# Performance work log

Hardware: AMD Instinct MI355X
Metric: run time of the kernel (lower is better)

The kernel has to match this reference:

```python
import jax, jax.numpy as jnp
import numpy as np

B, S, D = 2, 2048, 1024
H, HD = 16, 64  # num heads, head dim
EPS = 1e-12
SCALING = HD ** -0.5


def rotate_half(x):
    x1, x2 = jnp.split(x, 2, axis=-1)
    return jnp.concatenate([-x2, x1], axis=-1)


def setup_inputs() -> dict:
    key = jax.random.key(0)
    ks = jax.random.split(key, 12)
    hidden_states = jax.random.normal(ks[0], (B, S, D), dtype=jnp.float32)
    # RoPE tables (standard rotate-half convention)
    inv_freq = 1.0 / (10000.0 ** (np.arange(0, HD, 2, dtype=np.float32) / HD))
    pos = np.arange(S, dtype=np.float32)
    freqs = np.outer(pos, inv_freq)  # [S, HD/2]
    emb = np.concatenate([freqs, freqs], axis=-1)  # [S, HD]
    cos = jnp.asarray(np.cos(emb))
    sin = jnp.asarray(np.sin(emb))
    w = 0.02
    return {
        "hidden_states": hidden_states,
        "cos": cos,
        "sin": sin,
        "Wq": jax.random.normal(ks[1], (D, D), dtype=jnp.float32) * w,
        "bq": jnp.zeros((D,), dtype=jnp.float32),
        "Wk": jax.random.normal(ks[2], (D, D), dtype=jnp.float32) * w,
        "bk": jnp.zeros((D,), dtype=jnp.float32),
        "Wv": jax.random.normal(ks[3], (D, D), dtype=jnp.float32) * w,
        "bv": jnp.zeros((D,), dtype=jnp.float32),
        "Wo": jax.random.normal(ks[4], (D, D), dtype=jnp.float32) * w,
        "bo": jnp.zeros((D,), dtype=jnp.float32),
        "ln_w": jnp.ones((D,), dtype=jnp.float32),
        "ln_b": jnp.zeros((D,), dtype=jnp.float32),
    }


def reference(hidden_states, cos, sin, Wq, bq, Wk, bk, Wv, bv, Wo, bo, ln_w, ln_b):
    b, s, d = hidden_states.shape
    # QKV projections -> [b, h, s, hd]
    def proj(W, bias):
        return (hidden_states @ W.T + bias).reshape(b, s, H, HD).transpose(0, 2, 1, 3)
    q, k, v = proj(Wq, bq), proj(Wk, bk), proj(Wv, bv)
    # RoPE (cos/sin broadcast over batch and head dims)
    c = cos[None, None, :, :]
    sn = sin[None, None, :, :]
    q = q * c + rotate_half(q) * sn
    k = k * c + rotate_half(k) * sn
    # Faithful to source: query pre-scaled AND scaling applied inside attention
    q = q * SCALING
    scores = jnp.einsum("bhsd,bhtd->bhst", q, k) * SCALING
    attn = jax.nn.softmax(scores, axis=-1)
    ctx = jnp.einsum("bhst,bhtd->bhsd", attn, v)  # [b,h,s,hd]
    ctx = ctx.transpose(0, 2, 1, 3).reshape(b, s, d)
    # output dense + residual + LayerNorm
    out = ctx @ Wo.T + bo + hidden_states
    mu = jnp.mean(out, axis=-1, keepdims=True)
    var = jnp.var(out, axis=-1, keepdims=True)
    return (out - mu) / jnp.sqrt(var + EPS) * ln_w + ln_b
```

## Files before the change

### kernel.cpp

```cpp
#include <hip/hip_runtime.h>
#include <hip/hip_bf16.h>
#include <stdint.h>


typedef unsigned short ushort_t;
typedef short bf16x8 __attribute__((ext_vector_type(8)));
typedef float f32x4 __attribute__((ext_vector_type(4)));
typedef float f32x16 __attribute__((ext_vector_type(16)));
typedef unsigned short ushort8 __attribute__((ext_vector_type(8)));

#define LOG2E 1.4426950408889634f

__device__ __forceinline__ ushort_t f2b(float f) {
  uint32_t x = __builtin_bit_cast(uint32_t, f);
  return (ushort_t)((x + 0x7FFFu + ((x >> 16) & 1u)) >> 16);
}

__device__ __forceinline__ uint32_t cvt_pk_bf16(float lo, float hi) {
  uint32_t r;
  asm("v_cvt_pk_bf16_f32 %0, %1, %2" : "=v"(r) : "v"(lo), "v"(hi));
  return r;
}

__device__ __forceinline__ void permswap(uint32_t& a, uint32_t& b) {
  asm volatile("v_permlane32_swap_b32 %0, %1" : "+v"(a), "+v"(b));
}

__device__ __forceinline__ void gload16(const void* gptr, void* ldsptr) {
  __builtin_amdgcn_global_load_lds(
      (const __attribute__((address_space(1))) uint32_t*)gptr,
      (__attribute__((address_space(3))) uint32_t*)ldsptr, 16, 0, 0);
}

__global__ void cast_kernel(const float* __restrict__ src, ushort_t* __restrict__ dst, int n) {
  int i = (blockIdx.x * 256 + threadIdx.x) * 8;
  if (i >= n) return;
  const float4* s = (const float4*)(src + i);
  float4 a = s[0], b = s[1];
  ushort8 o = { f2b(a.x), f2b(a.y), f2b(a.z), f2b(a.w),
                f2b(b.x), f2b(b.y), f2b(b.z), f2b(b.w) };
  *(ushort8*)(dst + i) = o;
}

__global__ void cast4_kernel(const float* __restrict__ a, const float* __restrict__ b,
                             const float* __restrict__ c, const float* __restrict__ d2,
                             ushort_t* __restrict__ oa, ushort_t* __restrict__ ob,
                             ushort_t* __restrict__ oc, ushort_t* __restrict__ od) {
  const int which = blockIdx.x >> 9;
  const float* src = which == 0 ? a : which == 1 ? b : which == 2 ? c : d2;
  ushort_t* dst = which == 0 ? oa : which == 1 ? ob : which == 2 ? oc : od;
  int i = ((blockIdx.x & 511) * 256 + threadIdx.x) * 8;
  const float4* s = (const float4*)(src + i);
  float4 x = s[0], y = s[1];
  ushort8 o = { f2b(x.x), f2b(x.y), f2b(x.z), f2b(x.w),
                f2b(y.x), f2b(y.y), f2b(y.z), f2b(y.w) };
  *(ushort8*)(dst + i) = o;
}

__global__ __launch_bounds__(256) void gemm_qkv(
    const ushort_t* __restrict__ hid, const ushort_t* __restrict__ wq,
    const ushort_t* __restrict__ wk, const ushort_t* __restrict__ wv,
    const float* __restrict__ bq, const float* __restrict__ bk,
    const float* __restrict__ bv, const float* __restrict__ cosT,
    const float* __restrict__ sinT, ushort_t* __restrict__ qout,
    ushort_t* __restrict__ kout, ushort_t* __restrict__ vtout)
{
  constexpr int K = 1024;
  __shared__ uint4 As[512], Bs[512];
  const int which = blockIdx.z;
  const ushort_t* A;
  const ushort_t* Bm;
  const float* bias;
  int m0, n0;
  if (which == 0)      { A = hid; Bm = wq; bias = bq; m0 = blockIdx.x * 128; n0 = blockIdx.y * 128; }
  else if (which == 1) { A = hid; Bm = wk; bias = bk; m0 = blockIdx.x * 128; n0 = blockIdx.y * 128; }
  else                 { A = wv;  Bm = hid; bias = bv; m0 = blockIdx.y * 128; n0 = blockIdx.x * 128; }

  const int tid = threadIdx.x;
  const int wave = tid >> 6, lane = tid & 63;
  const int d = lane & 15, g = lane >> 4;
  const int wm = (wave >> 1) * 64, wn = (wave & 1) * 64;

  const ushort_t* ag = A + (size_t)(m0 + (tid >> 2)) * K + (tid & 3) * 8;
  const ushort_t* bg = Bm + (size_t)(n0 + (tid >> 2)) * K + (tid & 3) * 8;
  char* asd = (char*)As + wave * 1024;
  char* bsd = (char*)Bs + wave * 1024;

  f32x4 acc[4][4] = {};

  for (int k0 = 0; k0 < K; k0 += 32) {
    __syncthreads();
    gload16(ag + k0, asd);
    gload16(ag + 64 * K + k0, asd + 4096);
    gload16(bg + k0, bsd);
    gload16(bg + 64 * K + k0, bsd + 4096);
    __syncthreads();
    bf16x8 af[4], bfr[4];
#pragma unroll
    for (int i = 0; i < 4; ++i)
      af[i] = __builtin_bit_cast(bf16x8, As[(wm + i * 16 + d) * 4 + g]);
#pragma unroll
    for (int j = 0; j < 4; ++j)
      bfr[j] = __builtin_bit_cast(bf16x8, Bs[(wn + j * 16 + d) * 4 + g]);
#pragma unroll
    for (int i = 0; i < 4; ++i)
#pragma unroll
      for (int j = 0; j < 4; ++j)
        acc[i][j] = __builtin_amdgcn_mfma_f32_16x16x32_bf16(af[i], bfr[j], acc[i][j], 0, 0, 0);
  }

  if (which <= 1) {
    ushort_t* O = which == 0 ? qout : kout;
    const float qscale = which == 0 ? (LOG2E / 64.0f) : 1.0f;
    const int head_base = n0 + wn;
    const int h = head_base >> 6;
#pragma unroll
    for (int i = 0; i < 4; ++i) {
#pragma unroll
      for (int r = 0; r < 4; ++r) {
        const int m = m0 + wm + i * 16 + g * 4 + r;
        const int s = m & 2047, b = m >> 11;
#pragma unroll
        for (int j = 0; j < 4; ++j) {
          const int c = j * 16 + d;
          const float v0 = acc[i][j][r] + bias[head_base + c];
          const float v1 = acc[i][j ^ 2][r] + bias[head_base + (c ^ 32)];
          const float rot = (c < 32) ? -v1 : v1;
          const float vr = (v0 * cosT[s * 64 + c] + rot * sinT[s * 64 + c]) * qscale;
          O[(size_t)(((b << 4) + h) * 2048 + s) * 64 + c] = f2b(vr);
        }
      }
    }
  } else {
    ushort_t* O = vtout;
#pragma unroll
    for (int i = 0; i < 4; ++i) {
#pragma unroll
      for (int r = 0; r < 4; ++r) {
        const int fr = m0 + wm + i * 16 + g * 4 + r;
        const float bv2 = bias[fr];
        const int h = fr >> 6, dd = fr & 63;
#pragma unroll
        for (int j = 0; j < 4; ++j) {
          const int tok = n0 + wn + j * 16 + d;
          const int b = tok >> 11, s = tok & 2047;
          O[(size_t)(((b << 4) + h) * 64 + dd) * 2048 + s] = f2b(acc[i][j][r] + bv2);
        }
      }
    }
  }
}

__global__ __launch_bounds__(256) void gemm_wo(
    const ushort_t* __restrict__ A, const ushort_t* __restrict__ B,
    const float* __restrict__ bias, const float* __restrict__ resid,
    float* __restrict__ O)
{
  constexpr int K = 1024;
  __shared__ uint4 As[512], Bs[512];
  const int tid = threadIdx.x;
  const int wave = tid >> 6, lane = tid & 63;
  const int d = lane & 15, g = lane >> 4;
  const int m0 = blockIdx.x * 128, n0 = blockIdx.y * 128;
  const int wm = (wave >> 1) * 64, wn = (wave & 1) * 64;

  const ushort_t* ag = A + (size_t)(m0 + (tid >> 2)) * K + (tid & 3) * 8;
  const ushort_t* bg = B + (size_t)(n0 + (tid >> 2)) * K + (tid & 3) * 8;
  char* asd = (char*)As + wave * 1024;
  char* bsd = (char*)Bs + wave * 1024;

  f32x4 acc[4][4] = {};

  for (int k0 = 0; k0 < K; k0 += 32) {
    __syncthreads();
    gload16(ag + k0, asd);
    gload16(ag + 64 * K + k0, asd + 4096);
    gload16(bg + k0, bsd);
    gload16(bg + 64 * K + k0, bsd + 4096);
    __syncthreads();
    bf16x8 af[4], bfr[4];
#pragma unroll
    for (int i = 0; i < 4; ++i)
      af[i] = __builtin_bit_cast(bf16x8, As[(wm + i * 16 + d) * 4 + g]);
#pragma unroll
    for (int j = 0; j < 4; ++j)
      bfr[j] = __builtin_bit_cast(bf16x8, Bs[(wn + j * 16 + d) * 4 + g]);
#pragma unroll
    for (int i = 0; i < 4; ++i)
#pragma unroll
      for (int j = 0; j < 4; ++j)
        acc[i][j] = __builtin_amdgcn_mfma_f32_16x16x32_bf16(af[i], bfr[j], acc[i][j], 0, 0, 0);
  }

#pragma unroll
  for (int i = 0; i < 4; ++i)
#pragma unroll
    for (int r = 0; r < 4; ++r) {
      const int m = m0 + wm + i * 16 + g * 4 + r;
#pragma unroll
      for (int j = 0; j < 4; ++j) {
        const int n = n0 + wn + j * 16 + d;
        O[(size_t)m * 1024 + n] = acc[i][j][r] + bias[n] + resid[(size_t)m * 1024 + n];
      }
    }
}

__global__ __launch_bounds__(256, 2) void attn_kernel(
    const ushort_t* __restrict__ Q, const ushort_t* __restrict__ Kb,
    const ushort_t* __restrict__ VT, ushort_t* __restrict__ ctx)
{
  __shared__ uint4 KV[2048];
  const int orig = blockIdx.x;
  const int wgid = (orig & 7) * 64 + (orig >> 3);
  const int bh = wgid >> 4;
  const int q0 = (wgid & 15) * 128;
  const int tid = threadIdx.x, wave = tid >> 6, lane = tid & 63;
  const int ql = lane & 31, h2 = lane >> 5;
  const int qrow = q0 + wave * 32 + ql;

  bf16x8 qf[4];
  {
    const ushort_t* qp = Q + ((size_t)bh * 2048 + qrow) * 64 + h2 * 8;
#pragma unroll
    for (int s = 0; s < 4; ++s)
      qf[s] = __builtin_bit_cast(bf16x8, *(const uint4*)(qp + 16 * s));
  }

  const int st_row = tid >> 3, st_c8 = tid & 7;
  const ushort_t* kgp = Kb + (size_t)(bh * 2048 + st_row) * 64 + st_c8 * 8;
  const ushort_t* vgp = VT + (size_t)(bh * 64 + st_row) * 2048 + st_c8 * 8;
  const int sidx0 = st_row * 8 + (st_c8 ^ (st_row & 7));
  const int sidx1 = (st_row + 32) * 8 + (st_c8 ^ (st_row & 7));

  uint4 kr0 = *(const uint4*)(kgp);
  uint4 kr1 = *(const uint4*)(kgp + 32 * 64);
  uint4 vr0 = *(const uint4*)(vgp);
  uint4 vr1 = *(const uint4*)(vgp + 32 * 2048);
  KV[sidx0] = kr0; KV[sidx1] = kr1;
  KV[512 + sidx0] = vr0; KV[512 + sidx1] = vr1;
  __syncthreads();

  float lsum = 0.f;
  f32x16 cacc[2] = {};

  for (int t = 0; t < 32; ++t) {
    const int cb = (t & 1) << 10;
    const int nb = ((t + 1) & 1) << 10;
    const int kvn = (t + 1) * 64;
    if (t < 31) {
      kr0 = *(const uint4*)(kgp + kvn * 64);
      kr1 = *(const uint4*)(kgp + (kvn + 32) * 64);
      vr0 = *(const uint4*)(vgp + kvn);
      vr1 = *(const uint4*)(vgp + 32 * 2048 + kvn);
    }

    f32x16 sacc[2];
#pragma unroll
    for (int jj = 0; jj < 2; ++jj) {
      f32x16 z = {};
#pragma unroll
      for (int s = 0; s < 4; ++s) {
        bf16x8 kf = __builtin_bit_cast(bf16x8,
            KV[cb + (jj * 32 + ql) * 8 + ((2 * s + h2) ^ (ql & 7))]);
        z = __builtin_amdgcn_mfma_f32_32x32x16_bf16(kf, qf[s], z, 0, 0, 0);
      }
      sacc[jj] = z;
    }

    bf16x8 pf[4];
    float ps0 = 0.f, ps1 = 0.f;
#pragma unroll
    for (int s = 0; s < 4; ++s) {
      const int jj = s >> 1;
      const int rb = (s & 1) * 8;
      float p0 = __builtin_amdgcn_exp2f(sacc[jj][rb + 0]);
      float p1 = __builtin_amdgcn_exp2f(sacc[jj][rb + 1]);
      float p2 = __builtin_amdgcn_exp2f(sacc[jj][rb + 2]);
      float p3 = __builtin_amdgcn_exp2f(sacc[jj][rb + 3]);
      float p4 = __builtin_amdgcn_exp2f(sacc[jj][rb + 4]);
      float p5 = __builtin_amdgcn_exp2f(sacc[jj][rb + 5]);
      float p6 = __builtin_amdgcn_exp2f(sacc[jj][rb + 6]);
      float p7 = __builtin_amdgcn_exp2f(sacc[jj][rb + 7]);
      ps0 += (p0 + p1) + (p2 + p3);
      ps1 += (p4 + p5) + (p6 + p7);
      uint32_t a1 = cvt_pk_bf16(p0, p1);
      uint32_t a2 = cvt_pk_bf16(p2, p3);
      uint32_t b1 = cvt_pk_bf16(p4, p5);
      uint32_t b2 = cvt_pk_bf16(p6, p7);
      permswap(a1, b1);
      permswap(a2, b2);
      uint4 u = {a1, a2, b1, b2};
      pf[s] = __builtin_bit_cast(bf16x8, u);
    }
    lsum += ps0 + ps1;

#pragma unroll
    for (int dt = 0; dt < 2; ++dt)
#pragma unroll
      for (int s = 0; s < 4; ++s) {
        bf16x8 vf = __builtin_bit_cast(bf16x8,
            KV[cb + 512 + (dt * 32 + ql) * 8 + ((2 * s + h2) ^ (ql & 7))]);
        cacc[dt] = __builtin_amdgcn_mfma_f32_32x32x16_bf16(vf, pf[s], cacc[dt], 0, 0, 0);
      }

    if (t < 31) {
      KV[nb + sidx0] = kr0; KV[nb + sidx1] = kr1;
      KV[nb + 512 + sidx0] = vr0; KV[nb + 512 + sidx1] = vr1;
    }
    __syncthreads();
  }

  lsum += __shfl_xor(lsum, 32, 64);
  const float rinv = 1.0f / lsum;
  const int b = bh >> 4, h = bh & 15;
  ushort_t* cp = ctx + ((size_t)(b * 2048 + qrow)) * 1024 + h * 64 + h2 * 4;
#pragma unroll
  for (int dt = 0; dt < 2; ++dt)
#pragma unroll
    for (int t = 0; t < 4; ++t) {
      uint2 w;
      w.x = cvt_pk_bf16(cacc[dt][4 * t + 0] * rinv, cacc[dt][4 * t + 1] * rinv);
      w.y = cvt_pk_bf16(cacc[dt][4 * t + 2] * rinv, cacc[dt][4 * t + 3] * rinv);
      *(uint2*)(cp + dt * 32 + t * 8) = w;
    }
}

__global__ __launch_bounds__(256) void ln_kernel(const float* __restrict__ x,
    const float* __restrict__ w, const float* __restrict__ b2, float* __restrict__ out)
{
  const int row = blockIdx.x, tid = threadIdx.x;
  const float4 v = ((const float4*)(x + (size_t)row * 1024))[tid];
  float s = v.x + v.y + v.z + v.w;
  float ss = v.x * v.x + v.y * v.y + v.z * v.z + v.w * v.w;
#pragma unroll
  for (int off = 32; off > 0; off >>= 1) {
    s += __shfl_down(s, off, 64);
    ss += __shfl_down(ss, off, 64);
  }
  __shared__ float red[8];
  if ((tid & 63) == 0) { red[tid >> 6] = s; red[4 + (tid >> 6)] = ss; }
  __syncthreads();
  const float S = red[0] + red[1] + red[2] + red[3];
  const float SS = red[4] + red[5] + red[6] + red[7];
  const float mu = S * (1.f / 1024.f);
  const float rstd = rsqrtf(SS * (1.f / 1024.f) - mu * mu + 1e-12f);
  const int c = tid * 4;
  float4 o;
  o.x = (v.x - mu) * rstd * w[c + 0] + b2[c + 0];
  o.y = (v.y - mu) * rstd * w[c + 1] + b2[c + 1];
  o.z = (v.z - mu) * rstd * w[c + 2] + b2[c + 2];
  o.w = (v.w - mu) * rstd * w[c + 3] + b2[c + 3];
  ((float4*)(out + (size_t)row * 1024))[tid] = o;
}

extern "C" void kernel_launch(void* const* d_in, const int* in_sizes, int n_in,
                              void* d_out, int out_size, void* d_ws, size_t ws_size,
                              hipStream_t stream) {
  const float* hidden = (const float*)d_in[0];
  const float* cosT = (const float*)d_in[1];
  const float* sinT = (const float*)d_in[2];
  const float* Wq = (const float*)d_in[3];
  const float* bq = (const float*)d_in[4];
  const float* Wk = (const float*)d_in[5];
  const float* bk = (const float*)d_in[6];
  const float* Wv = (const float*)d_in[7];
  const float* bv = (const float*)d_in[8];
  const float* Wo = (const float*)d_in[9];
  const float* bo = (const float*)d_in[10];
  const float* lnw = (const float*)d_in[11];
  const float* lnb = (const float*)d_in[12];

  char* ws = (char*)d_ws;
  const size_t MB = 1u << 20;
  ushort_t* hid_bf = (ushort_t*)(ws);
  ushort_t* wq_bf = (ushort_t*)(ws + 8 * MB);
  ushort_t* wk_bf = (ushort_t*)(ws + 10 * MB);
  ushort_t* wv_bf = (ushort_t*)(ws + 12 * MB);
  ushort_t* wo_bf = (ushort_t*)(ws + 14 * MB);
  ushort_t* q_buf = (ushort_t*)(ws + 16 * MB);
  ushort_t* k_buf = (ushort_t*)(ws + 24 * MB);
  ushort_t* vt_buf = (ushort_t*)(ws + 32 * MB);
  ushort_t* ctx_bf = (ushort_t*)(ws + 40 * MB);
  float* out_pre = (float*)(ws + 16 * MB);

  cast_kernel<<<2048, 256, 0, stream>>>(hidden, hid_bf, 4194304);
  cast4_kernel<<<2048, 256, 0, stream>>>(Wq, Wk, Wv, Wo, wq_bf, wk_bf, wv_bf, wo_bf);

  gemm_qkv<<<dim3(32, 8, 3), 256, 0, stream>>>(hid_bf, wq_bf, wk_bf, wv_bf,
                                               bq, bk, bv, cosT, sinT,
                                               q_buf, k_buf, vt_buf);
  attn_kernel<<<512, 256, 0, stream>>>(q_buf, k_buf, vt_buf, ctx_bf);
  gemm_wo<<<dim3(32, 8), 256, 0, stream>>>(ctx_bf, wo_bf, bo, hidden, out_pre);
  ln_kernel<<<4096, 256, 0, stream>>>(out_pre, lnw, lnb, (float*)d_out);
}
```

Baseline: 132.7 us.

## Double-buffer LDS tiles in QKV and output projection GEMMs

Doubles the shared-memory A/B tiles in both projection GEMMs and prefetches the next K-slice into the alternate buffer while MFMAs consume the current one. The loop now has a single barrier per iteration instead of two. The aim is to overlap global-to-LDS loads with matrix math and cut barrier stalls. In exchange, LDS use per block doubles, which can lower occupancy, and the barrier may still wait on the outstanding prefetch.

```diff
diff --git a/kernel.cpp b/kernel.cpp
--- a/kernel.cpp
+++ b/kernel.cpp
@@ -66,7 +66,7 @@
     ushort_t* __restrict__ kout, ushort_t* __restrict__ vtout)
 {
   constexpr int K = 1024;
-  __shared__ uint4 As[512], Bs[512];
+  __shared__ uint4 As[1024], Bs[1024];
   const int which = blockIdx.z;
   const ushort_t* A;
   const ushort_t* Bm;
@@ -83,31 +83,40 @@
 
   const ushort_t* ag = A + (size_t)(m0 + (tid >> 2)) * K + (tid & 3) * 8;
   const ushort_t* bg = Bm + (size_t)(n0 + (tid >> 2)) * K + (tid & 3) * 8;
-  char* asd = (char*)As + wave * 1024;
-  char* bsd = (char*)Bs + wave * 1024;
 
   f32x4 acc[4][4] = {};
 
-  for (int k0 = 0; k0 < K; k0 += 32) {
-    __syncthreads();
-    gload16(ag + k0, asd);
-    gload16(ag + 64 * K + k0, asd + 4096);
-    gload16(bg + k0, bsd);
-    gload16(bg + 64 * K + k0, bsd + 4096);
-    __syncthreads();
+#define STAGE_QKV(buf, k0)                                         \
+  {                                                                \
+    char* asd = (char*)(As + (buf) * 512) + wave * 1024;           \
+    char* bsd = (char*)(Bs + (buf) * 512) + wave * 1024;           \
+    gload16(ag + (k0), asd);                                       \
+    gload16(ag + 64 * K + (k0), asd + 4096);                       \
+    gload16(bg + (k0), bsd);                                       \
+    gload16(bg + 64 * K + (k0), bsd + 4096);                       \
+  }
+
+  STAGE_QKV(0, 0);
+  __syncthreads();
+
+  for (int t = 0; t < 32; ++t) {
+    const int cb = (t & 1) << 9;
+    if (t < 31) STAGE_QKV((t + 1) & 1, (t + 1) * 32);
     bf16x8 af[4], bfr[4];
 #pragma unroll
     for (int i = 0; i < 4; ++i)
-      af[i] = __builtin_bit_cast(bf16x8, As[(wm + i * 16 + d) * 4 + g]);
+      af[i] = __builtin_bit_cast(bf16x8, As[cb + (wm + i * 16 + d) * 4 + g]);
 #pragma unroll
     for (int j = 0; j < 4; ++j)
-      bfr[j] = __builtin_bit_cast(bf16x8, Bs[(wn + j * 16 + d) * 4 + g]);
+      bfr[j] = __builtin_bit_cast(bf16x8, Bs[cb + (wn + j * 16 + d) * 4 + g]);
 #pragma unroll
     for (int i = 0; i < 4; ++i)
 #pragma unroll
       for (int j = 0; j < 4; ++j)
         acc[i][j] = __builtin_amdgcn_mfma_f32_16x16x32_bf16(af[i], bfr[j], acc[i][j], 0, 0, 0);
-  }
+    __syncthreads();
+  }
+#undef STAGE_QKV
 
   if (which <= 1) {
     ushort_t* O = which == 0 ? qout : kout;
@@ -157,7 +166,7 @@
     float* __restrict__ O)
 {
   constexpr int K = 1024;
-  __shared__ uint4 As[512], Bs[512];
+  __shared__ uint4 As[1024], Bs[1024];
   const int tid = threadIdx.x;
   const int wave = tid >> 6, lane = tid & 63;
   const int d = lane & 15, g = lane >> 4;
@@ -166,31 +175,40 @@
 
   const ushort_t* ag = A + (size_t)(m0 + (tid >> 2)) * K + (tid & 3) * 8;
   const ushort_t* bg = B + (size_t)(n0 + (tid >> 2)) * K + (tid & 3) * 8;
-  char* asd = (char*)As + wave * 1024;
-  char* bsd = (char*)Bs + wave * 1024;
 
   f32x4 acc[4][4] = {};
 
-  for (int k0 = 0; k0 < K; k0 += 32) {
-    __syncthreads();
-    gload16(ag + k0, asd);
-    gload16(ag + 64 * K + k0, asd + 4096);
-    gload16(bg + k0, bsd);
-    gload16(bg + 64 * K + k0, bsd + 4096);
-    __syncthreads();
+#define STAGE_WO(buf, k0)                                          \
+  {                                                                \
+    char* asd = (char*)(As + (buf) * 512) + wave * 1024;           \
+    char* bsd = (char*)(Bs + (buf) * 512) + wave * 1024;           \
+    gload16(ag + (k0), asd);                                       \
+    gload16(ag + 64 * K + (k0), asd + 4096);                       \
+    gload16(bg + (k0), bsd);                                       \
+    gload16(bg + 64 * K + (k0), bsd + 4096);                       \
+  }
+
+  STAGE_WO(0, 0);
+  __syncthreads();
+
+  for (int t = 0; t < 32; ++t) {
+    const int cb = (t & 1) << 9;
+    if (t < 31) STAGE_WO((t + 1) & 1, (t + 1) * 32);
     bf16x8 af[4], bfr[4];
 #pragma unroll
     for (int i = 0; i < 4; ++i)
-      af[i] = __builtin_bit_cast(bf16x8, As[(wm + i * 16 + d) * 4 + g]);
+      af[i] = __builtin_bit_cast(bf16x8, As[cb + (wm + i * 16 + d) * 4 + g]);
 #pragma unroll
     for (int j = 0; j < 4; ++j)
-      bfr[j] = __builtin_bit_cast(bf16x8, Bs[(wn + j * 16 + d) * 4 + g]);
+      bfr[j] = __builtin_bit_cast(bf16x8, Bs[cb + (wn + j * 16 + d) * 4 + g]);
 #pragma unroll
     for (int i = 0; i < 4; ++i)
 #pragma unroll
       for (int j = 0; j < 4; ++j)
         acc[i][j] = __builtin_amdgcn_mfma_f32_16x16x32_bf16(af[i], bfr[j], acc[i][j], 0, 0, 0);
-  }
+    __syncthreads();
+  }
+#undef STAGE_WO
 
 #pragma unroll
   for (int i = 0; i < 4; ++i)
```

Measured after the change: 144.3 us. 1.09x slower.

## Triple-buffer LDS in QKV and output GEMMs to overlap loads with MFMA

Applied to the files above, without the earlier changes.

Replaces the single-buffered load-sync-compute loop in both GEMM kernels with a three-stage LDS ring. Global-to-LDS loads run two K-steps ahead, and waits use vmcnt counters with one barrier per iteration instead of two __syncthreads. The aim is to hide global memory latency behind MFMA work. In exchange, LDS use per block rises to 48KB, which may limit occupancy, and the correctness of the hand-written waitcnt sequencing has to hold.

```diff
diff --git a/kernel.cpp b/kernel.cpp
--- a/kernel.cpp
+++ b/kernel.cpp
@@ -66,7 +66,7 @@
     ushort_t* __restrict__ kout, ushort_t* __restrict__ vtout)
 {
   constexpr int K = 1024;
-  __shared__ uint4 As[512], Bs[512];
+  __shared__ uint4 SB[3072];
   const int which = blockIdx.z;
   const ushort_t* A;
   const ushort_t* Bm;
@@ -83,31 +83,54 @@
 
   const ushort_t* ag = A + (size_t)(m0 + (tid >> 2)) * K + (tid & 3) * 8;
   const ushort_t* bg = Bm + (size_t)(n0 + (tid >> 2)) * K + (tid & 3) * 8;
-  char* asd = (char*)As + wave * 1024;
-  char* bsd = (char*)Bs + wave * 1024;
 
   f32x4 acc[4][4] = {};
 
-  for (int k0 = 0; k0 < K; k0 += 32) {
-    __syncthreads();
-    gload16(ag + k0, asd);
-    gload16(ag + 64 * K + k0, asd + 4096);
-    gload16(bg + k0, bsd);
-    gload16(bg + 64 * K + k0, bsd + 4096);
-    __syncthreads();
-    bf16x8 af[4], bfr[4];
-#pragma unroll
-    for (int i = 0; i < 4; ++i)
-      af[i] = __builtin_bit_cast(bf16x8, As[(wm + i * 16 + d) * 4 + g]);
-#pragma unroll
-    for (int j = 0; j < 4; ++j)
-      bfr[j] = __builtin_bit_cast(bf16x8, Bs[(wn + j * 16 + d) * 4 + g]);
-#pragma unroll
-    for (int i = 0; i < 4; ++i)
-#pragma unroll
-      for (int j = 0; j < 4; ++j)
-        acc[i][j] = __builtin_amdgcn_mfma_f32_16x16x32_bf16(af[i], bfr[j], acc[i][j], 0, 0, 0);
-  }
+#define STAGE_Q(buf, k0)                                           \
+  {                                                                \
+    char* dst = (char*)SB + (buf) * 16384 + wave * 1024;           \
+    gload16(ag + (k0), dst);                                       \
+    gload16(ag + 64 * K + (k0), dst + 4096);                       \
+    gload16(bg + (k0), dst + 8192);                                \
+    gload16(bg + 64 * K + (k0), dst + 12288);                      \
+  }
+
+#define COMPUTE_Q(buf)                                                          \
+  {                                                                             \
+    bf16x8 af[4], bfr[4];                                                       \
+    _Pragma("unroll") for (int i = 0; i < 4; ++i)                               \
+        af[i] = __builtin_bit_cast(bf16x8,                                      \
+            SB[(buf) * 1024 + (wm + i * 16 + d) * 4 + g]);                      \
+    _Pragma("unroll") for (int j = 0; j < 4; ++j)                               \
+        bfr[j] = __builtin_bit_cast(bf16x8,                                     \
+            SB[(buf) * 1024 + 512 + (wn + j * 16 + d) * 4 + g]);                \
+    _Pragma("unroll") for (int i = 0; i < 4; ++i)                               \
+        _Pragma("unroll") for (int j = 0; j < 4; ++j)                           \
+            acc[i][j] = __builtin_amdgcn_mfma_f32_16x16x32_bf16(                \
+                af[i], bfr[j], acc[i][j], 0, 0, 0);                             \
+  }
+
+  STAGE_Q(0, 0);
+  STAGE_Q(1, 32);
+  asm volatile("s_waitcnt vmcnt(4)" ::: "memory");
+  __builtin_amdgcn_s_barrier();
+
+  int bufc = 0;
+  for (int t = 0; t < 30; ++t) {
+    int bufn = bufc + 2; if (bufn >= 3) bufn -= 3;
+    STAGE_Q(bufn, (t + 2) * 32);
+    COMPUTE_Q(bufc);
+    asm volatile("s_waitcnt vmcnt(4)" ::: "memory");
+    __builtin_amdgcn_s_barrier();
+    bufc = (bufc == 2) ? 0 : bufc + 1;
+  }
+  COMPUTE_Q(bufc);
+  asm volatile("s_waitcnt vmcnt(0)" ::: "memory");
+  __builtin_amdgcn_s_barrier();
+  bufc = (bufc == 2) ? 0 : bufc + 1;
+  COMPUTE_Q(bufc);
+#undef STAGE_Q
+#undef COMPUTE_Q
 
   if (which <= 1) {
     ushort_t* O = which == 0 ? qout : kout;
@@ -157,7 +180,7 @@
     float* __restrict__ O)
 {
   constexpr int K = 1024;
-  __shared__ uint4 As[512], Bs[512];
+  __shared__ uint4 SB[3072];
   const int tid = threadIdx.x;
   const int wave = tid >> 6, lane = tid & 63;
   const int d = lane & 15, g = lane >> 4;
@@ -166,31 +189,54 @@
 
   const ushort_t* ag = A + (size_t)(m0 + (tid >> 2)) * K + (tid & 3) * 8;
   const ushort_t* bg = B + (size_t)(n0 + (tid >> 2)) * K + (tid & 3) * 8;
-  char* asd = (char*)As + wave * 1024;
-  char* bsd = (char*)Bs + wave * 1024;
 
   f32x4 acc[4][4] = {};
 
-  for (int k0 = 0; k0 < K; k0 += 32) {
-    __syncthreads();
-    gload16(ag + k0, asd);
-    gload16(ag + 64 * K + k0, asd + 4096);
-    gload16(bg + k0, bsd);
-    gload16(bg + 64 * K + k0, bsd + 4096);
-    __syncthreads();
-    bf16x8 af[4], bfr[4];
-#pragma unroll
-    for (int i = 0; i < 4; ++i)
-      af[i] = __builtin_bit_cast(bf16x8, As[(wm + i * 16 + d) * 4 + g]);
-#pragma unroll
-    for (int j = 0; j < 4; ++j)
-      bfr[j] = __builtin_bit_cast(bf16x8, Bs[(wn + j * 16 + d) * 4 + g]);
-#pragma unroll
-    for (int i = 0; i < 4; ++i)
-#pragma unroll
-      for (int j = 0; j < 4; ++j)
-        acc[i][j] = __builtin_amdgcn_mfma_f32_16x16x32_bf16(af[i], bfr[j], acc[i][j], 0, 0, 0);
-  }
+#define STAGE_W(buf, k0)                                           \
+  {                                                                \
+    char* dst = (char*)SB + (buf) * 16384 + wave * 1024;           \
+    gload16(ag + (k0), dst);                                       \
+    gload16(ag + 64 * K + (k0), dst + 4096);                       \
+    gload16(bg + (k0), dst + 8192);                                \
+    gload16(bg + 64 * K + (k0), dst + 12288);                      \
+  }
+
+#define COMPUTE_W(buf)                                                          \
+  {                                                                             \
+    bf16x8 af[4], bfr[4];                                                       \
+    _Pragma("unroll") for (int i = 0; i < 4; ++i)                               \
+        af[i] = __builtin_bit_cast(bf16x8,                                      \
+            SB[(buf) * 1024 + (wm + i * 16 + d) * 4 + g]);                      \
+    _Pragma("unroll") for (int j = 0; j < 4; ++j)                               \
+        bfr[j] = __builtin_bit_cast(bf16x8,                                     \
+            SB[(buf) * 1024 + 512 + (wn + j * 16 + d) * 4 + g]);                \
+    _Pragma("unroll") for (int i = 0; i < 4; ++i)                               \
+        _Pragma("unroll") for (int j = 0; j < 4; ++j)                           \
+            acc[i][j] = __builtin_amdgcn_mfma_f32_16x16x32_bf16(                \
+                af[i], bfr[j], acc[i][j], 0, 0, 0);                             \
+  }
+
+  STAGE_W(0, 0);
+  STAGE_W(1, 32);
+  asm volatile("s_waitcnt vmcnt(4)" ::: "memory");
+  __builtin_amdgcn_s_barrier();
+
+  int bufc = 0;
+  for (int t = 0; t < 30; ++t) {
+    int bufn = bufc + 2; if (bufn >= 3) bufn -= 3;
+    STAGE_W(bufn, (t + 2) * 32);
+    COMPUTE_W(bufc);
+    asm volatile("s_waitcnt vmcnt(4)" ::: "memory");
+    __builtin_amdgcn_s_barrier();
+    bufc = (bufc == 2) ? 0 : bufc + 1;
+  }
+  COMPUTE_W(bufc);
+  asm volatile("s_waitcnt vmcnt(0)" ::: "memory");
+  __builtin_amdgcn_s_barrier();
+  bufc = (bufc == 2) ? 0 : bufc + 1;
+  COMPUTE_W(bufc);
+#undef STAGE_W
+#undef COMPUTE_W
 
 #pragma unroll
   for (int i = 0; i < 4; ++i)
```

After: 114.0 us. -14.1%, faster.
